# Optimization experiments

Hardware: AMD Instinct MI355X
Metric: run time of the kernel (lower is better)

The kernel has to match this reference:

```python
import jax, jax.numpy as jnp
import numpy as np

N = 100000
E = 1600000
F_NODE = 6
F_EDGE = 2
H = 64


def _glorot(key, shape):
    lim = float(np.sqrt(6.0 / (shape[0] + shape[1])))
    return jax.random.uniform(key, shape, jnp.float32, -lim, lim)


def setup_inputs() -> dict:
    key = jax.random.key(0)
    ks = jax.random.split(key, 16)
    inp = {
        "x": jax.random.normal(ks[0], (N, F_NODE), jnp.float32),
        "edge_index": jax.random.randint(ks[1], (2, E), 0, N, jnp.int64),
        "edge_attr": jax.random.normal(ks[2], (E, F_EDGE), jnp.float32),
        # GCN layers (PyG GCNConv: linear no-bias, then aggregate, then +bias)
        "W1": _glorot(ks[3], (F_NODE, H)), "b1": jnp.zeros((H,), jnp.float32),
        "W2": _glorot(ks[4], (H, H)), "b2": jnp.zeros((H,), jnp.float32),
        "W3": _glorot(ks[5], (H, H)), "b3": jnp.zeros((H,), jnp.float32),
        # edge_mlp
        "We1": _glorot(ks[6], (F_EDGE, H)), "be1": jnp.zeros((H,), jnp.float32),
        "We2": _glorot(ks[7], (H, H)), "be2": jnp.zeros((H,), jnp.float32),
        # predictor
        "Wp1": _glorot(ks[8], (3 * H, H)), "bp1": jnp.zeros((H,), jnp.float32),
        "Wp2": _glorot(ks[9], (H, H // 2)), "bp2": jnp.zeros((H // 2,), jnp.float32),
        "Wp3": _glorot(ks[10], (H // 2, 1)), "bp3": jnp.zeros((1,), jnp.float32),
    }
    return inp


def _gcn_conv(h, W, b, src_sl, dst_sl, norm, n):
    # PyG GCNConv with self-loops and symmetric normalization
    h = h @ W                                   # [N, H_out]
    msg = h[src_sl] * norm[:, None]             # gather + scale per edge(+loop)
    out = jax.ops.segment_sum(msg, dst_sl, num_segments=n)
    return out + b


def _forward(x, edge_attr, W1, b1, W2, b2, W3, b3, We1, be1, We2, be2,
             Wp1, bp1, Wp2, bp2, Wp3, bp3, edge_index):
    n = x.shape[0]
    src, dst = edge_index[0], edge_index[1]

    # --- edge feature injection (vectorized version of per-edge loop) ---
    ef = jax.nn.relu(edge_attr @ We1 + be1) @ We2 + be2      # [E, H]
    nef = (jax.ops.segment_sum(ef, src, num_segments=n)
           + jax.ops.segment_sum(ef, dst, num_segments=n))   # [N, H]
    ones_e = jnp.ones((ef.shape[0],), x.dtype)
    deg = (jax.ops.segment_sum(ones_e, src, num_segments=n)
           + jax.ops.segment_sum(ones_e, dst, num_segments=n))
    deg = jnp.maximum(deg, 1.0)
    nef = nef / deg[:, None]
    # hidden_dim (64) >= node feature dim (6) -> truncate
    x = x + nef[:, : x.shape[1]] * 0.5

    # --- GCN normalization with self-loops (shared across layers) ---
    loop = jnp.arange(n, dtype=src.dtype)
    src_sl = jnp.concatenate([src, loop])
    dst_sl = jnp.concatenate([dst, loop])
    deg_sl = jax.ops.segment_sum(jnp.ones_like(dst_sl, dtype=x.dtype), dst_sl,
                                 num_segments=n)
    dinv = jnp.where(deg_sl > 0, deg_sl ** -0.5, 0.0)
    norm = dinv[src_sl] * dinv[dst_sl]

    h = jax.nn.relu(_gcn_conv(x, W1, b1, src_sl, dst_sl, norm, n))
    h = jax.nn.relu(_gcn_conv(h, W2, b2, src_sl, dst_sl, norm, n))
    h = _gcn_conv(h, W3, b3, src_sl, dst_sl, norm, n)

    graph_emb = h.mean(axis=0)                 # global_mean_pool, batch=None
    node_mean = h.mean(axis=0)
    node_std = jnp.std(h, axis=0, ddof=1)      # torch.std is unbiased
    combined = jnp.concatenate([graph_emb, node_mean, node_std])  # [3H]

    p = jax.nn.relu(combined @ Wp1 + bp1)      # dropout inactive in eval
    p = jax.nn.relu(p @ Wp2 + bp2)
    out = jax.nn.sigmoid(p @ Wp3 + bp3)        # (1,)
    return out


def reference(x, edge_index, edge_attr, W1, b1, W2, b2, W3, b3,
              We1, be1, We2, be2, Wp1, bp1, Wp2, bp2, Wp3, bp3):
    return _forward(x, edge_attr, W1, b1, W2, b2, W3, b3, We1, be1, We2, be2,
                    Wp1, bp1, Wp2, bp2, Wp3, bp3, edge_index)
```

## Files before the change

kernel.cpp:

```cpp
#include <hip/hip_runtime.h>
#include <hip/hip_bf16.h>
#include <stdint.h>

typedef float floatx2 __attribute__((ext_vector_type(2)));

__device__ __forceinline__ float rdlane(float v, int l) {
    return __uint_as_float(__builtin_amdgcn_readlane(__float_as_uint(v), l));
}
__device__ __forceinline__ float bf2f(unsigned short u) {
    return __uint_as_float(((unsigned)u) << 16);
}
__device__ __forceinline__ unsigned short f2bf(float f) {
    unsigned u = __float_as_uint(f);
    u += 0x7fffu + ((u >> 16) & 1u);
    return (unsigned short)(u >> 16);
}
__device__ __forceinline__ unsigned packbf(float a, float b) {
    return (unsigned)f2bf(a) | ((unsigned)f2bf(b) << 16);
}
__device__ __forceinline__ unsigned pk_fp8x4(float a, float b, float c, float d) {
    int u = __builtin_amdgcn_cvt_pk_fp8_f32(a, b, 0, false);
    u = __builtin_amdgcn_cvt_pk_fp8_f32(c, d, u, true);
    return (unsigned)u;
}

__global__ void k_zero(int* __restrict__ cntO, int* __restrict__ cntI,
                       double* __restrict__ sums, int n) {
    int i = blockIdx.x * blockDim.x + threadIdx.x;
    if (i < 128) sums[i] = 0.0;
    if (i < n) { cntO[i] = 0; cntI[i] = 0; }
}

__global__ __launch_bounds__(256) void k_front(
    const int* __restrict__ ei, const float* __restrict__ ea,
    const float* __restrict__ We1, const float* __restrict__ be1,
    const float* __restrict__ We2, const float* __restrict__ be2,
    unsigned* __restrict__ efp, int* __restrict__ cntO, int* __restrict__ cntI,
    int* __restrict__ rankS, int* __restrict__ rankD, int E) {
    __shared__ float sWe1[128], sbe1[64], sWe2[64 * 6], sbe2[6];
    int t = threadIdx.x;
    if (t < 128) sWe1[t] = We1[t];
    if (t < 64) {
        sbe1[t] = be1[t];
#pragma unroll
        for (int c = 0; c < 6; ++c) sWe2[t * 6 + c] = We2[t * 64 + c];
    }
    if (t < 6) sbe2[t] = be2[t];
    __syncthreads();

    int e = blockIdx.x * blockDim.x + t;
    if (e >= E) return;

    int s = ei[e], d = ei[E + e];
    int rs = atomicAdd(&cntO[s], 1);
    int rd = atomicAdd(&cntI[d], 1);

    float2 aa = ((const float2*)ea)[e];
    float a0 = aa.x, a1 = aa.y;
    float acc[6];
#pragma unroll
    for (int c = 0; c < 6; ++c) acc[c] = sbe2[c];
#pragma unroll
    for (int j = 0; j < 64; ++j) {
        float h = fmaf(a0, sWe1[j], fmaf(a1, sWe1[64 + j], sbe1[j]));
        h = fmaxf(h, 0.f);
#pragma unroll
        for (int c = 0; c < 6; ++c) acc[c] = fmaf(h, sWe2[j * 6 + c], acc[c]);
    }
    unsigned* q = efp + (size_t)e * 3;
    q[0] = packbf(acc[0], acc[1]);
    q[1] = packbf(acc[2], acc[3]);
    q[2] = packbf(acc[4], acc[5]);
    rankS[e] = rs;
    rankD[e] = rd;
}

__global__ __launch_bounds__(256) void k_scan1(const int* __restrict__ cntO,
                                               const int* __restrict__ cntI,
                                               int2* __restrict__ bsum, int n) {
    __shared__ int2 l[256];
    int i = blockIdx.x * 256 + threadIdx.x;
    l[threadIdx.x] = (i < n) ? make_int2(cntO[i], cntI[i]) : make_int2(0, 0);
    __syncthreads();
    for (int s = 128; s > 0; s >>= 1) {
        if (threadIdx.x < s) {
            l[threadIdx.x].x += l[threadIdx.x + s].x;
            l[threadIdx.x].y += l[threadIdx.x + s].y;
        }
        __syncthreads();
    }
    if (threadIdx.x == 0) bsum[blockIdx.x] = l[0];
}

__global__ __launch_bounds__(512) void k_scan2(int2* __restrict__ bsum, int nb,
                                               int* __restrict__ offON,
                                               int* __restrict__ offIN) {
    __shared__ int2 l[512];
    int t = threadIdx.x;
    int2 v = (t < nb) ? bsum[t] : make_int2(0, 0);
    l[t] = v;
    __syncthreads();
    for (int s = 1; s < 512; s <<= 1) {
        int2 tmp = (t >= s) ? l[t - s] : make_int2(0, 0);
        __syncthreads();
        l[t].x += tmp.x; l[t].y += tmp.y;
        __syncthreads();
    }
    if (t < nb) bsum[t] = make_int2(l[t].x - v.x, l[t].y - v.y);
    if (t == 511) { *offON = l[511].x; *offIN = l[511].y; }
}

__global__ __launch_bounds__(256) void k_scan3off(const int* __restrict__ cntO,
                                                  const int* __restrict__ cntI,
                                                  const int2* __restrict__ bsum,
                                                  int* __restrict__ offO,
                                                  int* __restrict__ offI, int n) {
    __shared__ int2 l[256];
    int i = blockIdx.x * 256 + threadIdx.x;
    int2 v = (i < n) ? make_int2(cntO[i], cntI[i]) : make_int2(0, 0);
    l[threadIdx.x] = v;
    __syncthreads();
    for (int s = 1; s < 256; s <<= 1) {
        int2 tmp = (threadIdx.x >= (unsigned)s) ? l[threadIdx.x - s] : make_int2(0, 0);
        __syncthreads();
        l[threadIdx.x].x += tmp.x; l[threadIdx.x].y += tmp.y;
        __syncthreads();
    }
    if (i < n) {
        int2 bs = bsum[blockIdx.x];
        offO[i] = l[threadIdx.x].x - v.x + bs.x;
        offI[i] = l[threadIdx.x].y - v.y + bs.y;
    }
}

__global__ __launch_bounds__(256) void k_place(const int* __restrict__ ei,
                                               const int* __restrict__ rankS,
                                               const int* __restrict__ rankD,
                                               const int* __restrict__ offO,
                                               const int* __restrict__ offI,
                                               const unsigned* __restrict__ efp,
                                               unsigned* __restrict__ out_rec,
                                               uint4* __restrict__ in_rec, int E) {
    int e = blockIdx.x * blockDim.x + threadIdx.x;
    if (e >= E) return;
    int s = ei[e], d = ei[E + e];
    const unsigned* q = efp + (size_t)e * 3;
    unsigned u0 = q[0], u1 = q[1], u2 = q[2];
    size_t so = (size_t)(offO[s] + rankS[e]) * 3;
    out_rec[so] = u0; out_rec[so + 1] = u1; out_rec[so + 2] = u2;
    in_rec[offI[d] + rankD[e]] = make_uint4((unsigned)s, u0, u1, u2);
}

__global__ __launch_bounds__(256) void k_nef_x(
    const int* __restrict__ offO, const unsigned* __restrict__ out_rec,
    const int* __restrict__ offI, const uint4* __restrict__ in_rec,
    const float* __restrict__ x,
    float* __restrict__ xp, float* __restrict__ dinv, int n) {
    int i = blockIdx.x * blockDim.x + threadIdx.x;
    if (i >= n) return;
    int bo = offO[i], eo = offO[i + 1];
    int bi = offI[i], eiN = offI[i + 1];
    float a0 = 0.f, a1 = 0.f, a2 = 0.f, a3 = 0.f, a4 = 0.f, a5 = 0.f;
    for (int j = bo; j < eo; ++j) {
        const unsigned* q = out_rec + (size_t)j * 3;
        unsigned u0 = q[0], u1 = q[1], u2 = q[2];
        a0 += bf2f((unsigned short)u0); a1 += bf2f((unsigned short)(u0 >> 16));
        a2 += bf2f((unsigned short)u1); a3 += bf2f((unsigned short)(u1 >> 16));
        a4 += bf2f((unsigned short)u2); a5 += bf2f((unsigned short)(u2 >> 16));
    }
    for (int j = bi; j < eiN; ++j) {
        uint4 r = in_rec[j];
        a0 += bf2f((unsigned short)r.y); a1 += bf2f((unsigned short)(r.y >> 16));
        a2 += bf2f((unsigned short)r.z); a3 += bf2f((unsigned short)(r.z >> 16));
        a4 += bf2f((unsigned short)r.w); a5 += bf2f((unsigned short)(r.w >> 16));
    }
    int indeg = eiN - bi;
    float degf = (float)((eo - bo) + indeg);
    float inv = 0.5f / fmaxf(degf, 1.f);
    xp[(size_t)i * 6 + 0] = x[(size_t)i * 6 + 0] + a0 * inv;
    xp[(size_t)i * 6 + 1] = x[(size_t)i * 6 + 1] + a1 * inv;
    xp[(size_t)i * 6 + 2] = x[(size_t)i * 6 + 2] + a2 * inv;
    xp[(size_t)i * 6 + 3] = x[(size_t)i * 6 + 3] + a3 * inv;
    xp[(size_t)i * 6 + 4] = x[(size_t)i * 6 + 4] + a4 * inv;
    xp[(size_t)i * 6 + 5] = x[(size_t)i * 6 + 5] + a5 * inv;
    dinv[i] = 1.f / sqrtf(1.f + (float)indeg);
}

__global__ __launch_bounds__(256) void k_mm1(const float* __restrict__ xp,
                                             const float* __restrict__ W1,
                                             const float* __restrict__ dinv,
                                             unsigned* __restrict__ sOut, int n) {
    int lane = threadIdx.x & 63;
    int sub = lane & 15;
    int wid = (blockIdx.x * blockDim.x + threadIdx.x) >> 6;
    int nw = (gridDim.x * blockDim.x) >> 6;
    float w[6];
#pragma unroll
    for (int c = 0; c < 6; ++c) w[c] = W1[c * 64 + lane];
    for (int i = wid; i < n; i += nw) {
        float xv = (lane < 6) ? xp[(size_t)i * 6 + lane] : 0.f;
        float acc = 0.f;
#pragma unroll
        for (int c = 0; c < 6; ++c) acc = fmaf(rdlane(xv, c), w[c], acc);
        float o = acc * dinv[i];
        float o0 = __shfl(o, sub * 4 + 0);
        float o1 = __shfl(o, sub * 4 + 1);
        float o2 = __shfl(o, sub * 4 + 2);
        float o3 = __shfl(o, sub * 4 + 3);
        if (lane < 16) sOut[(size_t)i * 16 + lane] = pk_fp8x4(o0, o1, o2, o3);
    }
}

__global__ __launch_bounds__(256) void k_gathermm(
    const int* __restrict__ offI, const uint4* __restrict__ in_rec,
    const float* __restrict__ dinv, const unsigned* __restrict__ sIn,
    const float* __restrict__ bias, const float* __restrict__ W,
    unsigned* __restrict__ sOut, int n) {
    int lane = threadIdx.x & 63;
    int sub = lane & 15, grp = lane >> 4;
    int wid = (blockIdx.x * blockDim.x + threadIdx.x) >> 6;
    int nw = (gridDim.x * blockDim.x) >> 6;
    float w[64];
#pragma unroll
    for (int c = 0; c < 64; ++c) w[c] = W[c * 64 + lane];
    float4 bb = ((const float4*)bias)[sub];

    for (int i = wid; i < n; i += nw) {
        unsigned su = sIn[(size_t)i * 16 + sub];
        float a0, a1, a2, a3;
        if (grp == 0) {
            floatx2 lo = __builtin_amdgcn_cvt_pk_f32_fp8(su, false);
            floatx2 hi = __builtin_amdgcn_cvt_pk_f32_fp8(su, true);
            a0 = lo.x; a1 = lo.y; a2 = hi.x; a3 = hi.y;
        } else { a0 = a1 = a2 = a3 = 0.f; }
        int b0 = offI[i], e0 = offI[i + 1];
#pragma unroll 4
        for (int j = b0 + grp; j < e0; j += 4) {
            unsigned src = in_rec[j].x;
            unsigned u = sIn[(size_t)src * 16 + sub];
            floatx2 lo = __builtin_amdgcn_cvt_pk_f32_fp8(u, false);
            floatx2 hi = __builtin_amdgcn_cvt_pk_f32_fp8(u, true);
            a0 += lo.x; a1 += lo.y; a2 += hi.x; a3 += hi.y;
        }
        a0 += __shfl_xor(a0, 16); a1 += __shfl_xor(a1, 16);
        a2 += __shfl_xor(a2, 16); a3 += __shfl_xor(a3, 16);
        a0 += __shfl_xor(a0, 32); a1 += __shfl_xor(a1, 32);
        a2 += __shfl_xor(a2, 32); a3 += __shfl_xor(a3, 32);

        float dv = dinv[i];
        float h0 = fmaxf(fmaf(a0, dv, bb.x), 0.f);
        float h1 = fmaxf(fmaf(a1, dv, bb.y), 0.f);
        float h2 = fmaxf(fmaf(a2, dv, bb.z), 0.f);
        float h3 = fmaxf(fmaf(a3, dv, bb.w), 0.f);
        float o = 0.f;
#pragma unroll
        for (int g = 0; g < 16; ++g) {
            o = fmaf(rdlane(h0, g), w[g * 4 + 0], o);
            o = fmaf(rdlane(h1, g), w[g * 4 + 1], o);
            o = fmaf(rdlane(h2, g), w[g * 4 + 2], o);
            o = fmaf(rdlane(h3, g), w[g * 4 + 3], o);
        }
        o *= dv;
        float o0 = __shfl(o, sub * 4 + 0);
        float o1 = __shfl(o, sub * 4 + 1);
        float o2 = __shfl(o, sub * 4 + 2);
        float o3 = __shfl(o, sub * 4 + 3);
        if (lane < 16) sOut[(size_t)i * 16 + lane] = pk_fp8x4(o0, o1, o2, o3);
    }
}

__global__ __launch_bounds__(256) void k_gatherreduce(
    const int* __restrict__ offI, const uint4* __restrict__ in_rec,
    const float* __restrict__ dinv, const unsigned* __restrict__ sIn,
    const float* __restrict__ b3, double* __restrict__ sums, int n) {
    int lane = threadIdx.x & 63;
    int sub = lane & 15, grp = lane >> 4;
    int wv = threadIdx.x >> 6;
    int wid = (blockIdx.x * blockDim.x + threadIdx.x) >> 6;
    int nw = (gridDim.x * blockDim.x) >> 6;
    float4 bb = ((const float4*)b3)[sub];
    double s0 = 0.0, s1 = 0.0, s2_ = 0.0, s3 = 0.0;
    double q0 = 0.0, q1 = 0.0, q2 = 0.0, q3 = 0.0;

    for (int i = wid; i < n; i += nw) {
        unsigned su = sIn[(size_t)i * 16 + sub];
        float a0, a1, a2, a3;
        if (grp == 0) {
            floatx2 lo = __builtin_amdgcn_cvt_pk_f32_fp8(su, false);
            floatx2 hi = __builtin_amdgcn_cvt_pk_f32_fp8(su, true);
            a0 = lo.x; a1 = lo.y; a2 = hi.x; a3 = hi.y;
        } else { a0 = a1 = a2 = a3 = 0.f; }
        int b0 = offI[i], e0 = offI[i + 1];
#pragma unroll 4
        for (int j = b0 + grp; j < e0; j += 4) {
            unsigned src = in_rec[j].x;
            unsigned u = sIn[(size_t)src * 16 + sub];
            floatx2 lo = __builtin_amdgcn_cvt_pk_f32_fp8(u, false);
            floatx2 hi = __builtin_amdgcn_cvt_pk_f32_fp8(u, true);
            a0 += lo.x; a1 += lo.y; a2 += hi.x; a3 += hi.y;
        }
        a0 += __shfl_xor(a0, 16); a1 += __shfl_xor(a1, 16);
        a2 += __shfl_xor(a2, 16); a3 += __shfl_xor(a3, 16);
        a0 += __shfl_xor(a0, 32); a1 += __shfl_xor(a1, 32);
        a2 += __shfl_xor(a2, 32); a3 += __shfl_xor(a3, 32);

        float dv = dinv[i];
        float v0 = fmaf(a0, dv, bb.x);
        float v1 = fmaf(a1, dv, bb.y);
        float v2 = fmaf(a2, dv, bb.z);
        float v3 = fmaf(a3, dv, bb.w);
        s0 += v0; s1 += v1; s2_ += v2; s3 += v3;
        q0 += (double)v0 * v0; q1 += (double)v1 * v1;
        q2 += (double)v2 * v2; q3 += (double)v3 * v3;
    }
    __shared__ double shS[4 * 64], shQ[4 * 64];
    if (grp == 0) {
#pragma unroll
        for (int k = 0; k < 4; ++k) {
            double sk = (k == 0) ? s0 : (k == 1) ? s1 : (k == 2) ? s2_ : s3;
            double qk = (k == 0) ? q0 : (k == 1) ? q1 : (k == 2) ? q2 : q3;
            shS[wv * 64 + sub * 4 + k] = sk;
            shQ[wv * 64 + sub * 4 + k] = qk;
        }
    }
    __syncthreads();
    if (wv == 0) {
        double a = shS[lane] + shS[64 + lane] + shS[128 + lane] + shS[192 + lane];
        double c = shQ[lane] + shQ[64 + lane] + shQ[128 + lane] + shQ[192 + lane];
        unsafeAtomicAdd(&sums[lane], a);
        unsafeAtomicAdd(&sums[64 + lane], c);
    }
}

__global__ void k_head(const double* __restrict__ sums,
                       const float* __restrict__ Wp1, const float* __restrict__ bp1,
                       const float* __restrict__ Wp2, const float* __restrict__ bp2,
                       const float* __restrict__ Wp3, const float* __restrict__ bp3,
                       float* __restrict__ out, int n) {
    __shared__ float comb[192], p1[64], p2[32];
    int t = threadIdx.x;
    if (t < 64) {
        double s = sums[t], s2 = sums[64 + t];
        double m = s / n;
        double var = (s2 - s * s / n) / (double)(n - 1);
        float mf = (float)m;
        float sd = (float)sqrt(var > 0.0 ? var : 0.0);
        comb[t] = mf;
        comb[64 + t] = mf;
        comb[128 + t] = sd;
    }
    __syncthreads();
    if (t < 64) {
        float acc = bp1[t];
        for (int k = 0; k < 192; ++k) acc = fmaf(comb[k], Wp1[k * 64 + t], acc);
        p1[t] = fmaxf(acc, 0.f);
    }
    __syncthreads();
    if (t < 32) {
        float acc = bp2[t];
        for (int k = 0; k < 64; ++k) acc = fmaf(p1[k], Wp2[k * 32 + t], acc);
        p2[t] = fmaxf(acc, 0.f);
    }
    __syncthreads();
    if (t == 0) {
        float acc = bp3[0];
        for (int k = 0; k < 32; ++k) acc = fmaf(p2[k], Wp3[k], acc);
        out[0] = 1.f / (1.f + expf(-acc));
    }
}

static inline char* align16(char* p) {
    return (char*)(((uintptr_t)p + 15) & ~(uintptr_t)15);
}

extern "C" void kernel_launch(void* const* d_in, const int* in_sizes, int n_in,
                              void* d_out, int out_size, void* d_ws, size_t ws_size,
                              hipStream_t stream) {
    const float* x   = (const float*)d_in[0];
    const int*   ei  = (const int*)d_in[1];
    const float* ea  = (const float*)d_in[2];
    const float* W1  = (const float*)d_in[3];
    const float* b1  = (const float*)d_in[4];
    const float* W2  = (const float*)d_in[5];
    const float* b2  = (const float*)d_in[6];
    const float* W3  = (const float*)d_in[7];
    const float* b3  = (const float*)d_in[8];
    const float* We1 = (const float*)d_in[9];
    const float* be1 = (const float*)d_in[10];
    const float* We2 = (const float*)d_in[11];
    const float* be2 = (const float*)d_in[12];
    const float* Wp1 = (const float*)d_in[13];
    const float* bp1 = (const float*)d_in[14];
    const float* Wp2 = (const float*)d_in[15];
    const float* bp2 = (const float*)d_in[16];
    const float* Wp3 = (const float*)d_in[17];
    const float* bp3 = (const float*)d_in[18];

    const int N = in_sizes[0] / 6;
    const int E = in_sizes[1] / 2;
    const int nbN = (N + 255) / 256;
    const int nbE = (E + 255) / 256;
    const size_t SB = (size_t)N * 64;

    char* p = (char*)d_ws;
    double* sums = (double*)p;          p = align16(p + 128 * sizeof(double));
    int* cntO = (int*)p;                p = align16(p + (size_t)N * 4);
    int* cntI = (int*)p;                p = align16(p + (size_t)N * 4);
    int* offO = (int*)p;                p = align16(p + ((size_t)N + 1) * 4);
    int* offI = (int*)p;                p = align16(p + ((size_t)N + 1) * 4);
    int2* bsum = (int2*)p;              p = align16(p + 512 * 8);
    float* xp = (float*)p;              p = align16(p + (size_t)N * 6 * 4);
    float* dinv = (float*)p;            p = align16(p + (size_t)N * 4);
    uint4* in_rec = (uint4*)p;          p = align16(p + (size_t)E * 16);
    char* u1 = p;                       p = align16(p + 2 * ((SB + 15) & ~(size_t)15));
    int* rankS = (int*)u1;
    int* rankD = (int*)(u1 + ((SB + 15) & ~(size_t)15));
    unsigned* sbufA = (unsigned*)rankS;
    unsigned* sbufB = (unsigned*)rankD;
    char* u2 = p;
    unsigned* efp = (unsigned*)u2;
    unsigned* out_rec = (unsigned*)(u2 + (size_t)E * 12);

    const int TB = 256;
    dim3 blk(TB);

    k_zero<<<dim3(nbN), blk, 0, stream>>>(cntO, cntI, sums, N);
    k_front<<<dim3(nbE), blk, 0, stream>>>(ei, ea, We1, be1, We2, be2,
                                           efp, cntO, cntI, rankS, rankD, E);
    k_scan1<<<dim3(nbN), blk, 0, stream>>>(cntO, cntI, bsum, N);
    k_scan2<<<dim3(1), dim3(512), 0, stream>>>(bsum, nbN, offO + N, offI + N);
    k_scan3off<<<dim3(nbN), blk, 0, stream>>>(cntO, cntI, bsum, offO, offI, N);
    k_place<<<dim3(nbE), blk, 0, stream>>>(ei, rankS, rankD, offO, offI, efp,
                                           out_rec, in_rec, E);
    k_nef_x<<<dim3(nbN), blk, 0, stream>>>(offO, out_rec, offI, in_rec, x, xp, dinv, N);

    k_mm1<<<dim3(1024), blk, 0, stream>>>(xp, W1, dinv, sbufA, N);
    k_gathermm<<<dim3(2048), blk, 0, stream>>>(offI, in_rec, dinv, sbufA, b1, W2, sbufB, N);
    k_gathermm<<<dim3(2048), blk, 0, stream>>>(offI, in_rec, dinv, sbufB, b2, W3, sbufA, N);
    k_gatherreduce<<<dim3(2048), blk, 0, stream>>>(offI, in_rec, dinv, sbufA, b3, sums, N);
    k_head<<<dim3(1), dim3(64), 0, stream>>>(sums, Wp1, bp1, Wp2, bp2, Wp3, bp3,
                                             (float*)d_out, N);
}
```

Baseline: 543.8 us.

## Replace per-node atomic CSR build with two-pass bucketed radix partition

```diff
diff --git a/kernel.cpp b/kernel.cpp
--- a/kernel.cpp
+++ b/kernel.cpp
@@ -4,41 +4,116 @@
 
 typedef float floatx2 __attribute__((ext_vector_type(2)));
 
+#define NPB 256
+#define NB 391
+#define NBLKA 512
+
 __device__ __forceinline__ float rdlane(float v, int l) {
     return __uint_as_float(__builtin_amdgcn_readlane(__float_as_uint(v), l));
-}
-__device__ __forceinline__ float bf2f(unsigned short u) {
-    return __uint_as_float(((unsigned)u) << 16);
-}
-__device__ __forceinline__ unsigned short f2bf(float f) {
-    unsigned u = __float_as_uint(f);
-    u += 0x7fffu + ((u >> 16) & 1u);
-    return (unsigned short)(u >> 16);
-}
-__device__ __forceinline__ unsigned packbf(float a, float b) {
-    return (unsigned)f2bf(a) | ((unsigned)f2bf(b) << 16);
 }
 __device__ __forceinline__ unsigned pk_fp8x4(float a, float b, float c, float d) {
     int u = __builtin_amdgcn_cvt_pk_fp8_f32(a, b, 0, false);
     u = __builtin_amdgcn_cvt_pk_fp8_f32(c, d, u, true);
     return (unsigned)u;
 }
-
-__global__ void k_zero(int* __restrict__ cntO, int* __restrict__ cntI,
-                       double* __restrict__ sums, int n) {
-    int i = blockIdx.x * blockDim.x + threadIdx.x;
-    if (i < 128) sums[i] = 0.0;
-    if (i < n) { cntO[i] = 0; cntI[i] = 0; }
-}
-
-__global__ __launch_bounds__(256) void k_front(
+__device__ __forceinline__ unsigned pk_fp8x2(float a, float b) {
+    return (unsigned)__builtin_amdgcn_cvt_pk_fp8_f32(a, b, 0, false);
+}
+
+__global__ __launch_bounds__(512) void k_zero(int* __restrict__ inTot,
+                                              double* __restrict__ sums) {
+    int t = threadIdx.x;
+    if (t < 128) sums[t] = 0.0;
+    if (t < NB) inTot[t] = 0;
+}
+
+__global__ __launch_bounds__(256) void k_A1(const int* __restrict__ ei,
+                                            int* __restrict__ h,
+                                            int* __restrict__ inTot,
+                                            int E, int epb) {
+    __shared__ int hist[NB], histIn[NB];
+    int t = threadIdx.x, blk = blockIdx.x;
+    for (int b = t; b < NB; b += 256) { hist[b] = 0; histIn[b] = 0; }
+    __syncthreads();
+    int e0 = blk * epb, e1 = min(E, e0 + epb);
+    for (int e = e0 + t; e < e1; e += 256) {
+        int s = ei[e], d = ei[E + e];
+        atomicAdd(&hist[s >> 8], 1);
+        atomicAdd(&hist[d >> 8], 1);
+        atomicAdd(&histIn[d >> 8], 1);
+    }
+    __syncthreads();
+    for (int b = t; b < NB; b += 256) {
+        h[(size_t)b * NBLKA + blk] = hist[b];
+        if (histIn[b]) atomicAdd(&inTot[b], histIn[b]);
+    }
+}
+
+__global__ __launch_bounds__(512) void k_sc1(const int* __restrict__ v,
+                                             int* __restrict__ bsum, int n) {
+    __shared__ int l[512];
+    int i = blockIdx.x * 512 + threadIdx.x;
+    l[threadIdx.x] = (i < n) ? v[i] : 0;
+    __syncthreads();
+    for (int s = 256; s > 0; s >>= 1) {
+        if (threadIdx.x < s) l[threadIdx.x] += l[threadIdx.x + s];
+        __syncthreads();
+    }
+    if (threadIdx.x == 0) bsum[blockIdx.x] = l[0];
+}
+__global__ __launch_bounds__(512) void k_sc2(int* __restrict__ bsum, int nb) {
+    __shared__ int l[512];
+    int t = threadIdx.x;
+    int v = (t < nb) ? bsum[t] : 0;
+    l[t] = v;
+    __syncthreads();
+    for (int s = 1; s < 512; s <<= 1) {
+        int tmp = (t >= s) ? l[t - s] : 0;
+        __syncthreads();
+        l[t] += tmp;
+        __syncthreads();
+    }
+    if (t < nb) bsum[t] = l[t] - v;
+}
+__global__ __launch_bounds__(512) void k_sc3(int* __restrict__ v,
+                                             const int* __restrict__ bsum, int n) {
+    __shared__ int l[512];
+    int i = blockIdx.x * 512 + threadIdx.x;
+    int x = (i < n) ? v[i] : 0;
+    l[threadIdx.x] = x;
+    __syncthreads();
+    for (int s = 1; s < 512; s <<= 1) {
+        int tmp = (threadIdx.x >= (unsigned)s) ? l[threadIdx.x - s] : 0;
+        __syncthreads();
+        l[threadIdx.x] += tmp;
+        __syncthreads();
+    }
+    if (i < n) v[i] = l[threadIdx.x] - x + bsum[blockIdx.x];
+}
+__global__ __launch_bounds__(512) void k_scanIn(const int* __restrict__ inTot,
+                                                int* __restrict__ inBase) {
+    __shared__ int l[512];
+    int t = threadIdx.x;
+    int v = (t < NB) ? inTot[t] : 0;
+    l[t] = v;
+    __syncthreads();
+    for (int s = 1; s < 512; s <<= 1) {
+        int tmp = (t >= s) ? l[t - s] : 0;
+        __syncthreads();
+        l[t] += tmp;
+        __syncthreads();
+    }
+    if (t < NB) inBase[t] = l[t] - v;
+}
+
+__global__ __launch_bounds__(256) void k_A2(
     const int* __restrict__ ei, const float* __restrict__ ea,
     const float* __restrict__ We1, const float* __restrict__ be1,
     const float* __restrict__ We2, const float* __restrict__ be2,
-    unsigned* __restrict__ efp, int* __restrict__ cntO, int* __restrict__ cntI,
-    int* __restrict__ rankS, int* __restrict__ rankD, int E) {
+    const int* __restrict__ hs, uint4* __restrict__ rec, int E, int epb) {
     __shared__ float sWe1[128], sbe1[64], sWe2[64 * 6], sbe2[6];
-    int t = threadIdx.x;
+    __shared__ int cur[NB];
+    int t = threadIdx.x, blk = blockIdx.x;
     if (t < 128) sWe1[t] = We1[t];
     if (t < 64) {
         sbe1[t] = be1[t];
@@ -46,144 +121,100 @@
         for (int c = 0; c < 6; ++c) sWe2[t * 6 + c] = We2[t * 64 + c];
     }
     if (t < 6) sbe2[t] = be2[t];
-    __syncthreads();
-
-    int e = blockIdx.x * blockDim.x + t;
-    if (e >= E) return;
-
-    int s = ei[e], d = ei[E + e];
-    int rs = atomicAdd(&cntO[s], 1);
-    int rd = atomicAdd(&cntI[d], 1);
-
-    float2 aa = ((const float2*)ea)[e];
-    float a0 = aa.x, a1 = aa.y;
-    float acc[6];
-#pragma unroll
-    for (int c = 0; c < 6; ++c) acc[c] = sbe2[c];
-#pragma unroll
-    for (int j = 0; j < 64; ++j) {
-        float h = fmaf(a0, sWe1[j], fmaf(a1, sWe1[64 + j], sbe1[j]));
-        h = fmaxf(h, 0.f);
-#pragma unroll
-        for (int c = 0; c < 6; ++c) acc[c] = fmaf(h, sWe2[j * 6 + c], acc[c]);
-    }
-    unsigned* q = efp + (size_t)e * 3;
-    q[0] = packbf(acc[0], acc[1]);
-    q[1] = packbf(acc[2], acc[3]);
-    q[2] = packbf(acc[4], acc[5]);
-    rankS[e] = rs;
-    rankD[e] = rd;
-}
-
-__global__ __launch_bounds__(256) void k_scan1(const int* __restrict__ cntO,
-                                               const int* __restrict__ cntI,
-                                               int2* __restrict__ bsum, int n) {
-    __shared__ int2 l[256];
-    int i = blockIdx.x * 256 + threadIdx.x;
-    l[threadIdx.x] = (i < n) ? make_int2(cntO[i], cntI[i]) : make_int2(0, 0);
-    __syncthreads();
-    for (int s = 128; s > 0; s >>= 1) {
-        if (threadIdx.x < s) {
-            l[threadIdx.x].x += l[threadIdx.x + s].x;
-            l[threadIdx.x].y += l[threadIdx.x + s].y;
-        }
-        __syncthreads();
-    }
-    if (threadIdx.x == 0) bsum[blockIdx.x] = l[0];
-}
-
-__global__ __launch_bounds__(512) void k_scan2(int2* __restrict__ bsum, int nb,
-                                               int* __restrict__ offON,
-                                               int* __restrict__ offIN) {
-    __shared__ int2 l[512];
-    int t = threadIdx.x;
-    int2 v = (t < nb) ? bsum[t] : make_int2(0, 0);
-    l[t] = v;
-    __syncthreads();
-    for (int s = 1; s < 512; s <<= 1) {
-        int2 tmp = (t >= s) ? l[t - s] : make_int2(0, 0);
-        __syncthreads();
-        l[t].x += tmp.x; l[t].y += tmp.y;
-        __syncthreads();
-    }
-    if (t < nb) bsum[t] = make_int2(l[t].x - v.x, l[t].y - v.y);
-    if (t == 511) { *offON = l[511].x; *offIN = l[511].y; }
-}
-
-__global__ __launch_bounds__(256) void k_scan3off(const int* __restrict__ cntO,
-                                                  const int* __restrict__ cntI,
-                                                  const int2* __restrict__ bsum,
-                                                  int* __restrict__ offO,
-                                                  int* __restrict__ offI, int n) {
-    __shared__ int2 l[256];
-    int i = blockIdx.x * 256 + threadIdx.x;
-    int2 v = (i < n) ? make_int2(cntO[i], cntI[i]) : make_int2(0, 0);
-    l[threadIdx.x] = v;
+    for (int b = t; b < NB; b += 256) cur[b] = hs[(size_t)b * NBLKA + blk];
+    __syncthreads();
+
+    int e0 = blk * epb, e1 = min(E, e0 + epb);
+    for (int e = e0 + t; e < e1; e += 256) {
+        int s = ei[e], d = ei[E + e];
+        float2 aa = ((const float2*)ea)[e];
+        float acc[6];
+#pragma unroll
+        for (int c = 0; c < 6; ++c) acc[c] = sbe2[c];
+#pragma unroll
+        for (int j = 0; j < 64; ++j) {
+            float hh = fmaf(aa.x, sWe1[j], fmaf(aa.y, sWe1[64 + j], sbe1[j]));
+            hh = fmaxf(hh, 0.f);
+#pragma unroll
+            for (int c = 0; c < 6; ++c) acc[c] = fmaf(hh, sWe2[j * 6 + c], acc[c]);
+        }
+        unsigned z = pk_fp8x4(acc[0], acc[1], acc[2], acc[3]);
+        unsigned w = pk_fp8x2(acc[4], acc[5]);
+        int p0 = atomicAdd(&cur[s >> 8], 1);
+        rec[p0] = make_uint4((unsigned)(s << 1), 0u, z, w);
+        int p1 = atomicAdd(&cur[d >> 8], 1);
+        rec[p1] = make_uint4((unsigned)(d << 1) | 1u, (unsigned)s, z, w);
+    }
+}
+
+__global__ __launch_bounds__(256) void k_B(
+    const uint4* __restrict__ rec, const int* __restrict__ hs,
+    const int* __restrict__ inBase, const float* __restrict__ x,
+    float* __restrict__ xp, float* __restrict__ dinv,
+    int* __restrict__ offI, int* __restrict__ in_src, int E, int N) {
+    __shared__ float nef[NPB * 6];
+    __shared__ int degAll[NPB], degIn[NPB], rnk[NPB], sc[NPB], exO[NPB];
+    int t = threadIdx.x, b = blockIdx.x;
+#pragma unroll
+    for (int c = 0; c < 6; ++c) nef[t * 6 + c] = 0.f;
+    degAll[t] = 0; degIn[t] = 0; rnk[t] = 0;
+    __syncthreads();
+
+    int rb = hs[(size_t)b * NBLKA];
+    int re = (b == NB - 1) ? 2 * E : hs[(size_t)(b + 1) * NBLKA];
+    for (int j = rb + t; j < re; j += 256) {
+        uint4 r = rec[j];
+        int l = (int)((r.x >> 1) & 255u);
+        atomicAdd(&degAll[l], 1);
+        if (r.x & 1u) atomicAdd(&degIn[l], 1);
+        floatx2 p01 = __builtin_amdgcn_cvt_pk_f32_fp8(r.z, false);
+        floatx2 p23 = __builtin_amdgcn_cvt_pk_f32_fp8(r.z, true);
+        floatx2 p45 = __builtin_amdgcn_cvt_pk_f32_fp8(r.w, false);
+        atomicAdd(&nef[l * 6 + 0], p01.x);
+        atomicAdd(&nef[l * 6 + 1], p01.y);
+        atomicAdd(&nef[l * 6 + 2], p23.x);
+        atomicAdd(&nef[l * 6 + 3], p23.y);
+        atomicAdd(&nef[l * 6 + 4], p45.x);
+        atomicAdd(&nef[l * 6 + 5], p45.y);
+    }
+    __syncthreads();
+
+    int v = degIn[t];
+    sc[t] = v;
     __syncthreads();
     for (int s = 1; s < 256; s <<= 1) {
-        int2 tmp = (threadIdx.x >= (unsigned)s) ? l[threadIdx.x - s] : make_int2(0, 0);
-        __syncthreads();
-        l[threadIdx.x].x += tmp.x; l[threadIdx.x].y += tmp.y;
-        __syncthreads();
-    }
-    if (i < n) {
-        int2 bs = bsum[blockIdx.x];
-        offO[i] = l[threadIdx.x].x - v.x + bs.x;
-        offI[i] = l[threadIdx.x].y - v.y + bs.y;
-    }
-}
-
-__global__ __launch_bounds__(256) void k_place(const int* __restrict__ ei,
-                                               const int* __restrict__ rankS,
-                                               const int* __restrict__ rankD,
-                                               const int* __restrict__ offO,
-                                               const int* __restrict__ offI,
-                                               const unsigned* __restrict__ efp,
-                                               unsigned* __restrict__ out_rec,
-                                               uint4* __restrict__ in_rec, int E) {
-    int e = blockIdx.x * blockDim.x + threadIdx.x;
-    if (e >= E) return;
-    int s = ei[e], d = ei[E + e];
-    const unsigned* q = efp + (size_t)e * 3;
-    unsigned u0 = q[0], u1 = q[1], u2 = q[2];
-    size_t so = (size_t)(offO[s] + rankS[e]) * 3;
-    out_rec[so] = u0; out_rec[so + 1] = u1; out_rec[so + 2] = u2;
-    in_rec[offI[d] + rankD[e]] = make_uint4((unsigned)s, u0, u1, u2);
-}
-
-__global__ __launch_bounds__(256) void k_nef_x(
-    const int* __restrict__ offO, const unsigned* __restrict__ out_rec,
-    const int* __restrict__ offI, const uint4* __restrict__ in_rec,
-    const float* __restrict__ x,
-    float* __restrict__ xp, float* __restrict__ dinv, int n) {
-    int i = blockIdx.x * blockDim.x + threadIdx.x;
-    if (i >= n) return;
-    int bo = offO[i], eo = offO[i + 1];
-    int bi = offI[i], eiN = offI[i + 1];
-    float a0 = 0.f, a1 = 0.f, a2 = 0.f, a3 = 0.f, a4 = 0.f, a5 = 0.f;
-    for (int j = bo; j < eo; ++j) {
-        const unsigned* q = out_rec + (size_t)j * 3;
-        unsigned u0 = q[0], u1 = q[1], u2 = q[2];
-        a0 += bf2f((unsigned short)u0); a1 += bf2f((unsigned short)(u0 >> 16));
-        a2 += bf2f((unsigned short)u1); a3 += bf2f((unsigned short)(u1 >> 16));
-        a4 += bf2f((unsigned short)u2); a5 += bf2f((unsigned short)(u2 >> 16));
-    }
-    for (int j = bi; j < eiN; ++j) {
-        uint4 r = in_rec[j];
-        a0 += bf2f((unsigned short)r.y); a1 += bf2f((unsigned short)(r.y >> 16));
-        a2 += bf2f((unsigned short)r.z); a3 += bf2f((unsigned short)(r.z >> 16));
-        a4 += bf2f((unsigned short)r.w); a5 += bf2f((unsigned short)(r.w >> 16));
-    }
-    int indeg = eiN - bi;
-    float degf = (float)((eo - bo) + indeg);
-    float inv = 0.5f / fmaxf(degf, 1.f);
-    xp[(size_t)i * 6 + 0] = x[(size_t)i * 6 + 0] + a0 * inv;
-    xp[(size_t)i * 6 + 1] = x[(size_t)i * 6 + 1] + a1 * inv;
-    xp[(size_t)i * 6 + 2] = x[(size_t)i * 6 + 2] + a2 * inv;
-    xp[(size_t)i * 6 + 3] = x[(size_t)i * 6 + 3] + a3 * inv;
-    xp[(size_t)i * 6 + 4] = x[(size_t)i * 6 + 4] + a4 * inv;
-    xp[(size_t)i * 6 + 5] = x[(size_t)i * 6 + 5] + a5 * inv;
-    dinv[i] = 1.f / sqrtf(1.f + (float)indeg);
+        int tmp = (t >= s) ? sc[t - s] : 0;
+        __syncthreads();
+        sc[t] += tmp;
+        __syncthreads();
+    }
+    exO[t] = sc[t] - v;
+    __syncthreads();
+
+    int node = b * NPB + t;
+    int ib = inBase[b];
+    if (node <= N) offI[node] = ib + exO[t];
+    if (node < N) {
+        float da = (float)degAll[t];
+        float inv = 0.5f / fmaxf(da, 1.f);
+        const float2* xr = (const float2*)(x + (size_t)node * 6);
+        float2 x01 = xr[0], x23 = xr[1], x45 = xr[2];
+        float2* xw = (float2*)(xp + (size_t)node * 6);
+        xw[0] = make_float2(x01.x + nef[t * 6 + 0] * inv, x01.y + nef[t * 6 + 1] * inv);
+        xw[1] = make_float2(x23.x + nef[t * 6 + 2] * inv, x23.y + nef[t * 6 + 3] * inv);
+        xw[2] = make_float2(x45.x + nef[t * 6 + 4] * inv, x45.y + nef[t * 6 + 5] * inv);
+        dinv[node] = 1.f / sqrtf(1.f + (float)degIn[t]);
+    }
+    __syncthreads();
+
+    for (int j = rb + t; j < re; j += 256) {
+        uint4 r = rec[j];
+        if (r.x & 1u) {
+            int l = (int)((r.x >> 1) & 255u);
+            int k = atomicAdd(&rnk[l], 1);
+            in_src[ib + exO[l] + k] = (int)r.y;
+        }
+    }
 }
 
 __global__ __launch_bounds__(256) void k_mm1(const float* __restrict__ xp,
@@ -212,7 +243,7 @@
 }
 
 __global__ __launch_bounds__(256) void k_gathermm(
-    const int* __restrict__ offI, const uint4* __restrict__ in_rec,
+    const int* __restrict__ offI, const int* __restrict__ in_src,
     const float* __restrict__ dinv, const unsigned* __restrict__ sIn,
     const float* __restrict__ bias, const float* __restrict__ W,
     unsigned* __restrict__ sOut, int n) {
@@ -236,7 +267,7 @@
         int b0 = offI[i], e0 = offI[i + 1];
 #pragma unroll 4
         for (int j = b0 + grp; j < e0; j += 4) {
-            unsigned src = in_rec[j].x;
+            unsigned src = (unsigned)in_src[j];
             unsigned u = sIn[(size_t)src * 16 + sub];
             floatx2 lo = __builtin_amdgcn_cvt_pk_f32_fp8(u, false);
             floatx2 hi = __builtin_amdgcn_cvt_pk_f32_fp8(u, true);
@@ -270,7 +301,7 @@
 }
 
 __global__ __launch_bounds__(256) void k_gatherreduce(
-    const int* __restrict__ offI, const uint4* __restrict__ in_rec,
+    const int* __restrict__ offI, const int* __restrict__ in_src,
     const float* __restrict__ dinv, const unsigned* __restrict__ sIn,
     const float* __restrict__ b3, double* __restrict__ sums, int n) {
     int lane = threadIdx.x & 63;
@@ -293,7 +324,7 @@
         int b0 = offI[i], e0 = offI[i + 1];
 #pragma unroll 4
         for (int j = b0 + grp; j < e0; j += 4) {
-            unsigned src = in_rec[j].x;
+            unsigned src = (unsigned)in_src[j];
             unsigned u = sIn[(size_t)src * 16 + sub];
             floatx2 lo = __builtin_amdgcn_cvt_pk_f32_fp8(u, false);
             floatx2 hi = __builtin_amdgcn_cvt_pk_f32_fp8(u, true);
@@ -398,46 +429,41 @@
 
     const int N = in_sizes[0] / 6;
     const int E = in_sizes[1] / 2;
-    const int nbN = (N + 255) / 256;
-    const int nbE = (E + 255) / 256;
+    const int epb = (E + NBLKA - 1) / NBLKA;
+    const int HSZ = NB * NBLKA;
+    const int nScan = (HSZ + 511) / 512;
     const size_t SB = (size_t)N * 64;
 
     char* p = (char*)d_ws;
     double* sums = (double*)p;          p = align16(p + 128 * sizeof(double));
-    int* cntO = (int*)p;                p = align16(p + (size_t)N * 4);
-    int* cntI = (int*)p;                p = align16(p + (size_t)N * 4);
-    int* offO = (int*)p;                p = align16(p + ((size_t)N + 1) * 4);
-    int* offI = (int*)p;                p = align16(p + ((size_t)N + 1) * 4);
-    int2* bsum = (int2*)p;              p = align16(p + 512 * 8);
+    int* inTot = (int*)p;               p = align16(p + NB * 4);
+    int* inBase = (int*)p;              p = align16(p + NB * 4);
+    int* bsum = (int*)p;                p = align16(p + 512 * 4);
+    int* h = (int*)p;                   p = align16(p + (size_t)HSZ * 4);
     float* xp = (float*)p;              p = align16(p + (size_t)N * 6 * 4);
     float* dinv = (float*)p;            p = align16(p + (size_t)N * 4);
-    uint4* in_rec = (uint4*)p;          p = align16(p + (size_t)E * 16);
-    char* u1 = p;                       p = align16(p + 2 * ((SB + 15) & ~(size_t)15));
-    int* rankS = (int*)u1;
-    int* rankD = (int*)(u1 + ((SB + 15) & ~(size_t)15));
-    unsigned* sbufA = (unsigned*)rankS;
-    unsigned* sbufB = (unsigned*)rankD;
-    char* u2 = p;
-    unsigned* efp = (unsigned*)u2;
-    unsigned* out_rec = (unsigned*)(u2 + (size_t)E * 12);
-
-    const int TB = 256;
-    dim3 blk(TB);
-
-    k_zero<<<dim3(nbN), blk, 0, stream>>>(cntO, cntI, sums, N);
-    k_front<<<dim3(nbE), blk, 0, stream>>>(ei, ea, We1, be1, We2, be2,
-                                           efp, cntO, cntI, rankS, rankD, E);
-    k_scan1<<<dim3(nbN), blk, 0, stream>>>(cntO, cntI, bsum, N);
-    k_scan2<<<dim3(1), dim3(512), 0, stream>>>(bsum, nbN, offO + N, offI + N);
-    k_scan3off<<<dim3(nbN), blk, 0, stream>>>(cntO, cntI, bsum, offO, offI, N);
-    k_place<<<dim3(nbE), blk, 0, stream>>>(ei, rankS, rankD, offO, offI, efp,
-                                           out_rec, in_rec, E);
-    k_nef_x<<<dim3(nbN), blk, 0, stream>>>(offO, out_rec, offI, in_rec, x, xp, dinv, N);
+    int* offI = (int*)p;                p = align16(p + ((size_t)N + 1) * 4);
+    int* in_src = (int*)p;              p = align16(p + (size_t)E * 4);
+    char* u = p;
+    uint4* rec = (uint4*)u;
+    unsigned* sbufA = (unsigned*)u;
+    unsigned* sbufB = (unsigned*)(u + ((SB + 15) & ~(size_t)15));
+
+    dim3 blk(256);
+
+    k_zero<<<dim3(1), dim3(512), 0, stream>>>(inTot, sums);
+    k_A1<<<dim3(NBLKA), blk, 0, stream>>>(ei, h, inTot, E, epb);
+    k_sc1<<<dim3(nScan), dim3(512), 0, stream>>>(h, bsum, HSZ);
+    k_sc2<<<dim3(1), dim3(512), 0, stream>>>(bsum, nScan);
+    k_sc3<<<dim3(nScan), dim3(512), 0, stream>>>(h, bsum, HSZ);
+    k_scanIn<<<dim3(1), dim3(512), 0, stream>>>(inTot, inBase);
+    k_A2<<<dim3(NBLKA), blk, 0, stream>>>(ei, ea, We1, be1, We2, be2, h, rec, E, epb);
+    k_B<<<dim3(NB), blk, 0, stream>>>(rec, h, inBase, x, xp, dinv, offI, in_src, E, N);
 
     k_mm1<<<dim3(1024), blk, 0, stream>>>(xp, W1, dinv, sbufA, N);
-    k_gathermm<<<dim3(2048), blk, 0, stream>>>(offI, in_rec, dinv, sbufA, b1, W2, sbufB, N);
-    k_gathermm<<<dim3(2048), blk, 0, stream>>>(offI, in_rec, dinv, sbufB, b2, W3, sbufA, N);
-    k_gatherreduce<<<dim3(2048), blk, 0, stream>>>(offI, in_rec, dinv, sbufA, b3, sums, N);
+    k_gathermm<<<dim3(2048), blk, 0, stream>>>(offI, in_src, dinv, sbufA, b1, W2, sbufB, N);
+    k_gathermm<<<dim3(2048), blk, 0, stream>>>(offI, in_src, dinv, sbufB, b2, W3, sbufA, N);
+    k_gatherreduce<<<dim3(2048), blk, 0, stream>>>(offI, in_src, dinv, sbufA, b3, sums, N);
     k_head<<<dim3(1), dim3(64), 0, stream>>>(sums, Wp1, bp1, Wp2, bp2, Wp3, bp3,
                                              (float*)d_out, N);
 }
```

After: 615.5 us. 13.2% more time.
